# Optimization experiments

Hardware: AMD Instinct MI355X
Metric: run time of the kernel (lower is better)

## Reference

```python
import jax, jax.numpy as jnp
import numpy as np

L, D, H, NP, PS, C, OUT, N = 8, 768, 12, 14, 16, 3, 1000, 32
DH = D // H
S = NP * NP + 1  # 197 tokens (cls + patches)
EPS = 1e-5


def pos_embeddings(seq_len, d):
    # result[i,j] = sin(i/10000^(j/d)) if j even else cos(i/10000^((j-1)/d))
    i = np.arange(seq_len)[:, None].astype(np.float64)
    j = np.arange(d)[None, :]
    ang = i / (10000.0 ** ((j - (j % 2)) / d))
    pe = np.where(j % 2 == 0, np.sin(ang), np.cos(ang))
    return jnp.asarray(pe, dtype=jnp.float32)


def setup_inputs() -> dict:
    key = jax.random.key(0)
    ks = jax.random.split(key, 16)
    s = 0.02
    return {
        'images': jax.random.normal(ks[0], (N, C, NP * PS, NP * PS), jnp.float32),
        'Wm': jax.random.normal(ks[1], (C * PS * PS, D), jnp.float32) * s,
        'bm': jnp.zeros((D,), jnp.float32),
        'cls_tok': jax.random.uniform(ks[2], (1, D), jnp.float32),
        'pos_emb': pos_embeddings(S, D),
        'ln1_w': jnp.ones((L, D), jnp.float32),
        'ln1_b': jnp.zeros((L, D), jnp.float32),
        'Wq': jax.random.normal(ks[3], (L, H, DH, DH), jnp.float32) * s,
        'bq': jnp.zeros((L, H, DH), jnp.float32),
        'Wk': jax.random.normal(ks[4], (L, H, DH, DH), jnp.float32) * s,
        'bk': jnp.zeros((L, H, DH), jnp.float32),
        'Wv': jax.random.normal(ks[5], (L, H, DH, DH), jnp.float32) * s,
        'bv': jnp.zeros((L, H, DH), jnp.float32),
        'ln2_w': jnp.ones((L, D), jnp.float32),
        'ln2_b': jnp.zeros((L, D), jnp.float32),
        'W1': jax.random.normal(ks[6], (L, D, 4 * D), jnp.float32) * s,
        'b1': jnp.zeros((L, 4 * D), jnp.float32),
        'W2': jax.random.normal(ks[7], (L, 4 * D, D), jnp.float32) * s,
        'b2': jnp.zeros((L, D), jnp.float32),
        'Wout': jax.random.normal(ks[8], (D, OUT), jnp.float32) * s,
        'bout': jnp.zeros((OUT,), jnp.float32),
    }


def layernorm(x, w, b):
    mu = x.mean(-1, keepdims=True)
    var = ((x - mu) ** 2).mean(-1, keepdims=True)
    return (x - mu) * jax.lax.rsqrt(var + EPS) * w + b


def vit_forward(images, Wm, bm, cls_tok, pos_emb, ln1_w, ln1_b, Wq, bq, Wk, bk, Wv, bv,
                ln2_w, ln2_b, W1, b1, W2, b2, Wout, bout):
    n = images.shape[0]
    # patchify: (n,c,h,w) -> (n, NP*NP, C*PS*PS), each patch flattened in (c,ph,pw) order
    patches = images.reshape(n, C, NP, PS, NP, PS).transpose(0, 2, 4, 1, 3, 5)
    patches = patches.reshape(n, NP * NP, C * PS * PS)
    tokens = patches @ Wm + bm                                   # [n, S-1, D]
    tokens = jnp.concatenate([jnp.broadcast_to(cls_tok, (n, 1, D)), tokens], axis=1)
    out = tokens + pos_emb                                       # [n, S, D]

    scale = 1.0 / jnp.sqrt(jnp.asarray(DH, jnp.float32))

    def block(x, p):
        l1w, l1b, wq, bq_, wk, bk_, wv, bv_, l2w, l2b, w1, b1_, w2, b2_ = p
        h = layernorm(x, l1w, l1b).reshape(n, S, H, DH)
        q = jnp.einsum('nshd,hde->nshe', h, wq) + bq_
        k = jnp.einsum('nshd,hde->nshe', h, wk) + bk_
        v = jnp.einsum('nshd,hde->nshe', h, wv) + bv_
        att = jax.nn.softmax(jnp.einsum('nshe,nthe->nhst', q, k) * scale, axis=-1)
        o = jnp.einsum('nhst,nthe->nshe', att, v).reshape(n, S, D)
        x = x + o
        h2 = layernorm(x, l2w, l2b)
        x = x + (jax.nn.gelu(h2 @ w1 + b1_, approximate=False) @ w2 + b2_)
        return x, None

    out, _ = jax.lax.scan(block, out, (ln1_w, ln1_b, Wq, bq, Wk, bk, Wv, bv,
                                       ln2_w, ln2_b, W1, b1, W2, b2))
    cls = out[:, 0]                                              # [n, D]
    return jax.nn.softmax(cls @ Wout + bout, axis=-1)            # [n, OUT]


def reference(images, Wm, bm, cls_tok, pos_emb, ln1_w, ln1_b, Wq, bq, Wk, bk, Wv, bv,
              ln2_w, ln2_b, W1, b1, W2, b2, Wout, bout):
    return vit_forward(images, Wm, bm, cls_tok, pos_emb, ln1_w, ln1_b, Wq, bq, Wk, bk,
                       Wv, bv, ln2_w, ln2_b, W1, b1, W2, b2, Wout, bout)
```

## Files before the change

kernel.cpp:

```cpp
#include <hip/hip_runtime.h>
#include <math.h>

#define N_ 32
#define S_ 197
#define D_ 768
#define H_ 12
#define L_ 8
#define FF_ 3072
#define MTOK (N_ * S_)
#define ND (N_ * S_ * D_)

typedef __attribute__((ext_vector_type(8))) short short8x;
typedef __attribute__((ext_vector_type(4))) float floatx4;
typedef unsigned short ushort_t;
typedef unsigned int uint_t;

__device__ __forceinline__ ushort_t f2bf_rn(float x) {
  uint_t u = __float_as_uint(x);
  uint_t r = (u + 0x7fff + ((u >> 16) & 1)) >> 16;
  return (ushort_t)r;
}
__device__ __forceinline__ float bf2f(ushort_t h) {
  return __uint_as_float(((uint_t)h) << 16);
}

__global__ __launch_bounds__(256) void patchify_kernel(const float* __restrict__ img,
                                                       ushort_t* __restrict__ phi,
                                                       ushort_t* __restrict__ plo) {
  int idx = blockIdx.x * 256 + threadIdx.x;
  if (idx >= 6272 * 768) return;
  int mp = idx / 768, kk = idx - mp * 768;
  int n = mp / 196, p = mp - n * 196;
  int py = p / 14, px = p - py * 14;
  int c = kk >> 8, r = kk & 255;
  int u = r >> 4, vv = r & 15;
  float val = img[((size_t)(n * 3 + c) * 224 + py * 16 + u) * 224 + px * 16 + vv];
  ushort_t hi = f2bf_rn(val);
  phi[idx] = hi;
  plo[idx] = f2bf_rn(val - bf2f(hi));
}

__global__ __launch_bounds__(256) void cls_init_kernel(const float* __restrict__ cls_tok,
                                                       const float* __restrict__ pos,
                                                       float* __restrict__ x) {
  int idx = blockIdx.x * 256 + threadIdx.x;
  int n = idx / 768, d = idx - n * 768;
  x[(size_t)n * S_ * D_ + d] = cls_tok[d] + pos[d];
}

__global__ __launch_bounds__(256) void wconvert_kernel(const float* __restrict__ W,
                                                       ushort_t* __restrict__ Thi,
                                                       ushort_t* __restrict__ Tlo, int K, int N) {
  __shared__ float T[32][36];
  int n0 = blockIdx.x * 32, k0 = blockIdx.y * 32;
  int t = threadIdx.x;
  int r = t >> 3, c4 = (t & 7) * 4;
  float4 v = *(const float4*)&W[(size_t)(k0 + r) * N + n0 + c4];
  T[c4 + 0][r] = v.x;
  T[c4 + 1][r] = v.y;
  T[c4 + 2][r] = v.z;
  T[c4 + 3][r] = v.w;
  __syncthreads();
  ushort4 hi, lo;
  float a;
  a = T[r][c4 + 0]; hi.x = f2bf_rn(a); lo.x = f2bf_rn(a - bf2f(hi.x));
  a = T[r][c4 + 1]; hi.y = f2bf_rn(a); lo.y = f2bf_rn(a - bf2f(hi.y));
  a = T[r][c4 + 2]; hi.z = f2bf_rn(a); lo.z = f2bf_rn(a - bf2f(hi.z));
  a = T[r][c4 + 3]; hi.w = f2bf_rn(a); lo.w = f2bf_rn(a - bf2f(hi.w));
  size_t o = (size_t)(n0 + r) * K + k0 + c4;
  *(ushort4*)&Thi[o] = hi;
  *(ushort4*)&Tlo[o] = lo;
}

#define EPI_PATCH 1
#define EPI_GELU 2
#define EPI_ATOM 3
#define LDST 40

template <int EPI, int KP>
__global__ __launch_bounds__(256) void gemm_mfma(
    const ushort_t* __restrict__ Ahi, const ushort_t* __restrict__ Alo,
    const ushort_t* __restrict__ Bhi, const ushort_t* __restrict__ Blo,
    const float* __restrict__ bias, float* __restrict__ Cf, ushort_t* __restrict__ Chi,
    ushort_t* __restrict__ Clo, int M, int K, int Nc, const float* __restrict__ pos) {
  __shared__ ushort_t As[2][128 * LDST];
  __shared__ ushort_t Bs[2][128 * LDST];
  int tid = threadIdx.x;
  int wave = tid >> 6, lane = tid & 63;
  int wr = (wave >> 1) * 64, wc = (wave & 1) * 64;
  int q = lane >> 4, l15 = lane & 15;
  int m0 = blockIdx.x * 128, n0 = blockIdx.y * 128;
  int kbeg = (KP > 1) ? blockIdx.z * (K / KP) : 0;
  int kend = kbeg + K / KP;

  floatx4 acc[4][4];
#pragma unroll
  for (int i = 0; i < 4; ++i)
#pragma unroll
    for (int j = 0; j < 4; ++j)
#pragma unroll
      for (int e = 0; e < 4; ++e) acc[i][j][e] = 0.f;

  int sr = tid >> 2;
  int kq = tid & 3;

  for (int k0 = kbeg; k0 < kend; k0 += 32) {
#pragma unroll
    for (int it = 0; it < 2; ++it) {
      int rr = it * 64 + sr;
      int gm = m0 + rr;
      if (gm > M - 1) gm = M - 1;
      size_t aoff = (size_t)gm * K + k0 + kq * 8;
      *(uint4*)&As[0][rr * LDST + kq * 8] = *(const uint4*)&Ahi[aoff];
      *(uint4*)&As[1][rr * LDST + kq * 8] = *(const uint4*)&Alo[aoff];
      size_t boff = (size_t)(n0 + rr) * K + k0 + kq * 8;
      *(uint4*)&Bs[0][rr * LDST + kq * 8] = *(const uint4*)&Bhi[boff];
      *(uint4*)&Bs[1][rr * LDST + kq * 8] = *(const uint4*)&Blo[boff];
    }
    __syncthreads();
    short8x ah[4], al[4], bh[4], bl[4];
    int abase = (wr + l15) * LDST + q * 8;
    int bbase = (wc + l15) * LDST + q * 8;
#pragma unroll
    for (int i = 0; i < 4; ++i) {
      ah[i] = *(const short8x*)&As[0][abase + i * 16 * LDST];
      al[i] = *(const short8x*)&As[1][abase + i * 16 * LDST];
      bh[i] = *(const short8x*)&Bs[0][bbase + i * 16 * LDST];
      bl[i] = *(const short8x*)&Bs[1][bbase + i * 16 * LDST];
    }
#pragma unroll
    for (int i = 0; i < 4; ++i)
#pragma unroll
      for (int j = 0; j < 4; ++j) {
        acc[i][j] = __builtin_amdgcn_mfma_f32_16x16x32_bf16(ah[i], bh[j], acc[i][j], 0, 0, 0);
        acc[i][j] = __builtin_amdgcn_mfma_f32_16x16x32_bf16(ah[i], bl[j], acc[i][j], 0, 0, 0);
        acc[i][j] = __builtin_amdgcn_mfma_f32_16x16x32_bf16(al[i], bh[j], acc[i][j], 0, 0, 0);
      }
    __syncthreads();
  }

#pragma unroll
  for (int i = 0; i < 4; ++i) {
#pragma unroll
    for (int j = 0; j < 4; ++j) {
      int col = n0 + wc + j * 16 + l15;
#pragma unroll
      for (int r4 = 0; r4 < 4; ++r4) {
        int gr = m0 + wr + i * 16 + q * 4 + r4;
        if (gr >= M) continue;
        if (EPI == EPI_ATOM) {
          float v = acc[i][j][r4];
          if (KP == 1 || blockIdx.z == 0) v += bias[col];
          unsafeAtomicAdd(&Cf[(size_t)gr * 768 + col], v);
        } else {
          float v = acc[i][j][r4] + bias[col];
          if (EPI == EPI_PATCH) {
            int n = gr / 196, t = gr - n * 196 + 1;
            Cf[((size_t)n * S_ + t) * 768 + col] = v + pos[(size_t)t * 768 + col];
          } else {
            float g = 0.5f * v * (1.f + erff(v * 0.70710678118654752f));
            ushort_t hi = f2bf_rn(g);
            size_t o = (size_t)gr * FF_ + col;
            Chi[o] = hi;
            Clo[o] = f2bf_rn(g - bf2f(hi));
          }
        }
      }
    }
  }
}

__global__ __launch_bounds__(256) void ln_kernel(const float* __restrict__ x,
                                                 ushort_t* __restrict__ hhi,
                                                 ushort_t* __restrict__ hlo,
                                                 const float* __restrict__ w,
                                                 const float* __restrict__ b) {
  int tok = blockIdx.x * 4 + (threadIdx.x >> 6);
  int lane = threadIdx.x & 63;
  const float* xr = x + (size_t)tok * 768;
  float4 v[3];
  float s = 0.f, s2 = 0.f;
#pragma unroll
  for (int i = 0; i < 3; ++i) {
    v[i] = *(const float4*)&xr[i * 256 + lane * 4];
    s += v[i].x + v[i].y + v[i].z + v[i].w;
    s2 += v[i].x * v[i].x + v[i].y * v[i].y + v[i].z * v[i].z + v[i].w * v[i].w;
  }
#pragma unroll
  for (int m = 32; m > 0; m >>= 1) { s += __shfl_xor(s, m, 64); s2 += __shfl_xor(s2, m, 64); }
  float mu = s * (1.f / 768.f);
  float var = s2 * (1.f / 768.f) - mu * mu;
  float rs = rsqrtf(var + 1e-5f);
#pragma unroll
  for (int i = 0; i < 3; ++i) {
    float4 wv = *(const float4*)&w[i * 256 + lane * 4];
    float4 bv = *(const float4*)&b[i * 256 + lane * 4];
    float o0 = (v[i].x - mu) * rs * wv.x + bv.x;
    float o1 = (v[i].y - mu) * rs * wv.y + bv.y;
    float o2 = (v[i].z - mu) * rs * wv.z + bv.z;
    float o3 = (v[i].w - mu) * rs * wv.w + bv.w;
    ushort4 oh, ol;
    oh.x = f2bf_rn(o0); ol.x = f2bf_rn(o0 - bf2f(oh.x));
    oh.y = f2bf_rn(o1); ol.y = f2bf_rn(o1 - bf2f(oh.y));
    oh.z = f2bf_rn(o2); ol.z = f2bf_rn(o2 - bf2f(oh.z));
    oh.w = f2bf_rn(o3); ol.w = f2bf_rn(o3 - bf2f(oh.w));
    size_t o = (size_t)tok * 768 + i * 256 + lane * 4;
    *(ushort4*)&hhi[o] = oh;
    *(ushort4*)&hlo[o] = ol;
  }
}

#define KSTR 72

__global__ __launch_bounds__(256) void qkv_mfma(
    const ushort_t* __restrict__ hhi, const ushort_t* __restrict__ hlo,
    const float* __restrict__ Wq, const float* __restrict__ Wk, const float* __restrict__ Wv,
    const float* __restrict__ bq, const float* __restrict__ bk, const float* __restrict__ bv,
    ushort_t* __restrict__ qhi, ushort_t* __restrict__ qlo, ushort_t* __restrict__ khi,
    ushort_t* __restrict__ klo, ushort_t* __restrict__ vhi, ushort_t* __restrict__ vlo) {
  __shared__ ushort_t As[2][128 * KSTR];
  __shared__ ushort_t Ws[2][64 * KSTR];
  int tid = threadIdx.x;
  int wave = tid >> 6, lane = tid & 63;
  int q = lane >> 4, l15 = lane & 15;
  int m0 = blockIdx.x * 128, h = blockIdx.y;
  int wm = wave >> 1, wj = wave & 1;

#pragma unroll
  for (int p = 0; p < 2; ++p) {
    const ushort_t* src = p == 0 ? hhi : hlo;
#pragma unroll
    for (int it = 0; it < 4; ++it) {
      int idx = it * 256 + tid;
      int r = idx >> 3, c = idx & 7;
      int gm = m0 + r;
      if (gm > MTOK - 1) gm = MTOK - 1;
      *(uint4*)&As[p][r * KSTR + c * 8] = *(const uint4*)&src[(size_t)gm * 768 + h * 64 + c * 8];
    }
  }

  const float* Wmat[3] = {Wq + (size_t)h * 4096, Wk + (size_t)h * 4096, Wv + (size_t)h * 4096};
  const float* Bmat[3] = {bq + h * 64, bk + h * 64, bv + h * 64};
  ushort_t* Ohi[3] = {qhi, khi, vhi};
  ushort_t* Olo[3] = {qlo, klo, vlo};

  for (int mat = 0; mat < 3; ++mat) {
    __syncthreads();
#pragma unroll
    for (int it = 0; it < 4; ++it) {
      int idx = it * 256 + tid;
      int r = idx >> 4, c4 = (idx & 15) * 4;
      float4 wv = *(const float4*)&Wmat[mat][r * 64 + c4];
      float vals[4] = {wv.x, wv.y, wv.z, wv.w};
#pragma unroll
      for (int i = 0; i < 4; ++i) {
        ushort_t hi = f2bf_rn(vals[i]);
        Ws[0][(c4 + i) * KSTR + r] = hi;
        Ws[1][(c4 + i) * KSTR + r] = f2bf_rn(vals[i] - bf2f(hi));
      }
    }
    __syncthreads();

    floatx4 acc[4][2];
#pragma unroll
    for (int i = 0; i < 4; ++i)
#pragma unroll
      for (int j = 0; j < 2; ++j)
#pragma unroll
        for (int e = 0; e < 4; ++e) acc[i][j][e] = 0.f;

#pragma unroll
    for (int ks = 0; ks < 2; ++ks) {
      short8x bh[2], bl[2];
#pragma unroll
      for (int j = 0; j < 2; ++j) {
        int bb = (wj * 32 + j * 16 + l15) * KSTR + ks * 32 + q * 8;
        bh[j] = *(const short8x*)&Ws[0][bb];
        bl[j] = *(const short8x*)&Ws[1][bb];
      }
#pragma unroll
      for (int i = 0; i < 4; ++i) {
        int ab = (wm * 64 + i * 16 + l15) * KSTR + ks * 32 + q * 8;
        short8x ah = *(const short8x*)&As[0][ab];
        short8x al = *(const short8x*)&As[1][ab];
#pragma unroll
        for (int j = 0; j < 2; ++j) {
          acc[i][j] = __builtin_amdgcn_mfma_f32_16x16x32_bf16(ah, bh[j], acc[i][j], 0, 0, 0);
          acc[i][j] = __builtin_amdgcn_mfma_f32_16x16x32_bf16(ah, bl[j], acc[i][j], 0, 0, 0);
          acc[i][j] = __builtin_amdgcn_mfma_f32_16x16x32_bf16(al, bh[j], acc[i][j], 0, 0, 0);
        }
      }
    }
#pragma unroll
    for (int i = 0; i < 4; ++i)
#pragma unroll
      for (int j = 0; j < 2; ++j) {
        int col = wj * 32 + j * 16 + l15;
        float bias = Bmat[mat][col];
#pragma unroll
        for (int r = 0; r < 4; ++r) {
          int tok = m0 + wm * 64 + i * 16 + q * 4 + r;
          if (tok >= MTOK) continue;
          float v = acc[i][j][r] + bias;
          ushort_t hi = f2bf_rn(v);
          size_t o = (size_t)tok * 768 + h * 64 + col;
          Ohi[mat][o] = hi;
          Olo[mat][o] = f2bf_rn(v - bf2f(hi));
        }
      }
  }
}

__global__ __launch_bounds__(256) void attn_mfma(
    const ushort_t* __restrict__ qhi, const ushort_t* __restrict__ qlo,
    const ushort_t* __restrict__ khi, const ushort_t* __restrict__ klo,
    const ushort_t* __restrict__ vhi, const ushort_t* __restrict__ vlo,
    float* __restrict__ X) {
  __shared__ ushort_t Qs[2][64 * KSTR];
  __shared__ ushort_t Ks[2][64 * KSTR];
  __shared__ ushort_t Vs[2][64 * KSTR];
  int tid = threadIdx.x;
  int wave = tid >> 6, lane = tid & 63;
  int q = lane >> 4, l15 = lane & 15;
  int qc = blockIdx.x, h = blockIdx.y, n = blockIdx.z;
  int q0 = qc * 64;
  int row0 = wave * 16;

#pragma unroll
  for (int p = 0; p < 2; ++p) {
    const ushort_t* src = p == 0 ? qhi : qlo;
#pragma unroll
    for (int it = 0; it < 2; ++it) {
      int idx = it * 256 + tid;
      int r = idx >> 3, c = idx & 7;
      int gr = q0 + r;
      if (gr > S_ - 1) gr = S_ - 1;
      *(uint4*)&Qs[p][r * KSTR + c * 8] =
          *(const uint4*)&src[((size_t)n * S_ + gr) * 768 + h * 64 + c * 8];
    }
  }
  __syncthreads();
  short8x qa_h[2], qa_l[2];
#pragma unroll
  for (int ks = 0; ks < 2; ++ks) {
    int ab = (row0 + l15) * KSTR + ks * 32 + q * 8;
    qa_h[ks] = *(const short8x*)&Qs[0][ab];
    qa_l[ks] = *(const short8x*)&Qs[1][ab];
  }

  float mrow[4], lrow[4];
  floatx4 oa[4];
#pragma unroll
  for (int r = 0; r < 4; ++r) { mrow[r] = -INFINITY; lrow[r] = 0.f; }
#pragma unroll
  for (int j = 0; j < 4; ++j)
#pragma unroll
    for (int e = 0; e < 4; ++e) oa[j][e] = 0.f;

  for (int t = 0; t < 4; ++t) {
    __syncthreads();
#pragma unroll
    for (int p = 0; p < 2; ++p) {
      const ushort_t* src = p == 0 ? khi : klo;
#pragma unroll
      for (int it = 0; it < 2; ++it) {
        int idx = it * 256 + tid;
        int r = idx >> 3, c = idx & 7;
        int gk = t * 64 + r;
        if (gk > S_ - 1) gk = S_ - 1;
        *(uint4*)&Ks[p][r * KSTR + c * 8] =
            *(const uint4*)&src[((size_t)n * S_ + gk) * 768 + h * 64 + c * 8];
      }
    }
    {
      int d = tid & 63, kg = tid >> 6;
#pragma unroll
      for (int p = 0; p < 2; ++p) {
        const ushort_t* src = p == 0 ? vhi : vlo;
#pragma unroll
        for (int k4 = 0; k4 < 4; ++k4) {
          ushort4 pk;
          ushort_t tmp[4];
#pragma unroll
          for (int i = 0; i < 4; ++i) {
            int gk = t * 64 + kg * 16 + k4 * 4 + i;
            if (gk > S_ - 1) gk = S_ - 1;
            tmp[i] = src[((size_t)n * S_ + gk) * 768 + h * 64 + d];
          }
          pk.x = tmp[0]; pk.y = tmp[1]; pk.z = tmp[2]; pk.w = tmp[3];
          *(ushort4*)&Vs[p][d * KSTR + kg * 16 + k4 * 4] = pk;
        }
      }
    }
    __syncthreads();

    floatx4 sc[4];
#pragma unroll
    for (int j = 0; j < 4; ++j) {
#pragma unroll
      for (int e = 0; e < 4; ++e) sc[j][e] = 0.f;
#pragma unroll
      for (int ks = 0; ks < 2; ++ks) {
        int bb = (j * 16 + l15) * KSTR + ks * 32 + q * 8;
        short8x kb_h = *(const short8x*)&Ks[0][bb];
        short8x kb_l = *(const short8x*)&Ks[1][bb];
        sc[j] = __builtin_amdgcn_mfma_f32_16x16x32_bf16(qa_h[ks], kb_h, sc[j], 0, 0, 0);
        sc[j] = __builtin_amdgcn_mfma_f32_16x16x32_bf16(qa_h[ks], kb_l, sc[j], 0, 0, 0);
        sc[j] = __builtin_amdgcn_mfma_f32_16x16x32_bf16(qa_l[ks], kb_h, sc[j], 0, 0, 0);
      }
    }
    __syncthreads();

    bool kvalid[4];
#pragma unroll
    for (int j = 0; j < 4; ++j) kvalid[j] = (t * 64 + j * 16 + l15) < S_;
#pragma unroll
    for (int r = 0; r < 4; ++r) {
      float sv[4];
#pragma unroll
      for (int j = 0; j < 4; ++j) sv[j] = kvalid[j] ? sc[j][r] * 0.125f : -INFINITY;
      float mx = fmaxf(fmaxf(sv[0], sv[1]), fmaxf(sv[2], sv[3]));
#pragma unroll
      for (int msk = 1; msk < 16; msk <<= 1) mx = fmaxf(mx, __shfl_xor(mx, msk, 64));
      float mn = fmaxf(mrow[r], mx);
      float al = expf(mrow[r] - mn);
      float p[4], ps = 0.f;
#pragma unroll
      for (int j = 0; j < 4; ++j) { p[j] = expf(sv[j] - mn); ps += p[j]; }
#pragma unroll
      for (int msk = 1; msk < 16; msk <<= 1) ps += __shfl_xor(ps, msk, 64);
      lrow[r] = lrow[r] * al + ps;
      mrow[r] = mn;
#pragma unroll
      for (int j = 0; j < 4; ++j) oa[j][r] *= al;
      int prow = (row0 + q * 4 + r) * KSTR;
#pragma unroll
      for (int j = 0; j < 4; ++j) {
        ushort_t phv = f2bf_rn(p[j]);
        Ks[0][prow + j * 16 + l15] = phv;
        Ks[1][prow + j * 16 + l15] = f2bf_rn(p[j] - bf2f(phv));
      }
    }

#pragma unroll
    for (int ks = 0; ks < 2; ++ks) {
      int ab = (row0 + l15) * KSTR + ks * 32 + q * 8;
      short8x pa_h = *(const short8x*)&Ks[0][ab];
      short8x pa_l = *(const short8x*)&Ks[1][ab];
#pragma unroll
      for (int j = 0; j < 4; ++j) {
        int bb = (j * 16 + l15) * KSTR + ks * 32 + q * 8;
        short8x vb_h = *(const short8x*)&Vs[0][bb];
        short8x vb_l = *(const short8x*)&Vs[1][bb];
        oa[j] = __builtin_amdgcn_mfma_f32_16x16x32_bf16(pa_h, vb_h, oa[j], 0, 0, 0);
        oa[j] = __builtin_amdgcn_mfma_f32_16x16x32_bf16(pa_h, vb_l, oa[j], 0, 0, 0);
        oa[j] = __builtin_amdgcn_mfma_f32_16x16x32_bf16(pa_l, vb_h, oa[j], 0, 0, 0);
      }
    }
  }

#pragma unroll
  for (int r = 0; r < 4; ++r) {
    int row = q0 + row0 + q * 4 + r;
    if (row >= S_) continue;
    float invl = 1.f / lrow[r];
#pragma unroll
    for (int j = 0; j < 4; ++j)
      X[((size_t)n * S_ + row) * 768 + h * 64 + j * 16 + l15] += oa[j][r] * invl;
  }
}

__global__ __launch_bounds__(256) void head_kernel(const float* __restrict__ x,
                                                   const float* __restrict__ Wout,
                                                   const float* __restrict__ bout,
                                                   float* __restrict__ out) {
  __shared__ float cls[768];
  __shared__ float red[4];
  int n = blockIdx.x, tid = threadIdx.x;
  int w = tid >> 6, lane = tid & 63;
  for (int d = tid; d < 768; d += 256) cls[d] = x[(size_t)n * S_ * D_ + d];
  __syncthreads();
  int j0 = tid * 4;
  bool act = j0 < 1000;
  float a0 = 0.f, a1 = 0.f, a2 = 0.f, a3 = 0.f;
  if (act) {
    for (int kk = 0; kk < 768; ++kk) {
      float c = cls[kk];
      float4 wv = *(const float4*)&Wout[(size_t)kk * 1000 + j0];
      a0 += c * wv.x;
      a1 += c * wv.y;
      a2 += c * wv.z;
      a3 += c * wv.w;
    }
    a0 += bout[j0];
    a1 += bout[j0 + 1];
    a2 += bout[j0 + 2];
    a3 += bout[j0 + 3];
  }
  float mx = act ? fmaxf(fmaxf(a0, a1), fmaxf(a2, a3)) : -INFINITY;
#pragma unroll
  for (int m = 32; m > 0; m >>= 1) mx = fmaxf(mx, __shfl_xor(mx, m, 64));
  if (lane == 0) red[w] = mx;
  __syncthreads();
  mx = fmaxf(fmaxf(red[0], red[1]), fmaxf(red[2], red[3]));
  __syncthreads();
  float e0 = 0.f, e1 = 0.f, e2 = 0.f, e3 = 0.f, ss = 0.f;
  if (act) {
    e0 = expf(a0 - mx);
    e1 = expf(a1 - mx);
    e2 = expf(a2 - mx);
    e3 = expf(a3 - mx);
    ss = e0 + e1 + e2 + e3;
  }
#pragma unroll
  for (int m = 32; m > 0; m >>= 1) ss += __shfl_xor(ss, m, 64);
  if (lane == 0) red[w] = ss;
  __syncthreads();
  ss = red[0] + red[1] + red[2] + red[3];
  if (act) {
    float inv = 1.f / ss;
    out[(size_t)n * 1000 + j0] = e0 * inv;
    out[(size_t)n * 1000 + j0 + 1] = e1 * inv;
    out[(size_t)n * 1000 + j0 + 2] = e2 * inv;
    out[(size_t)n * 1000 + j0 + 3] = e3 * inv;
  }
}

extern "C" void kernel_launch(void* const* d_in, const int* in_sizes, int n_in, void* d_out,
                              int out_size, void* d_ws, size_t ws_size, hipStream_t stream) {
  const float* images = (const float*)d_in[0];
  const float* Wm = (const float*)d_in[1];
  const float* bm = (const float*)d_in[2];
  const float* cls_tok = (const float*)d_in[3];
  const float* pos_emb = (const float*)d_in[4];
  const float* ln1_w = (const float*)d_in[5];
  const float* ln1_b = (const float*)d_in[6];
  const float* Wq = (const float*)d_in[7];
  const float* bq = (const float*)d_in[8];
  const float* Wk = (const float*)d_in[9];
  const float* bk = (const float*)d_in[10];
  const float* Wv = (const float*)d_in[11];
  const float* bv = (const float*)d_in[12];
  const float* ln2_w = (const float*)d_in[13];
  const float* ln2_b = (const float*)d_in[14];
  const float* W1 = (const float*)d_in[15];
  const float* b1 = (const float*)d_in[16];
  const float* W2 = (const float*)d_in[17];
  const float* b2 = (const float*)d_in[18];
  const float* Wout = (const float*)d_in[19];
  const float* bout = (const float*)d_in[20];
  float* out = (float*)d_out;

  char* base = (char*)d_ws;
  float* x = (float*)base;
  ushort_t* hhi = (ushort_t*)(base + (size_t)ND * 4);
  ushort_t* hlo = hhi + (size_t)ND;
  char* R = base + (size_t)ND * 8;
  ushort_t* qhi = (ushort_t*)R;
  ushort_t* qlo = qhi + (size_t)ND;
  ushort_t* khi = qlo + (size_t)ND;
  ushort_t* klo = khi + (size_t)ND;
  ushort_t* vhi = klo + (size_t)ND;
  ushort_t* vlo = vhi + (size_t)ND;
  ushort_t* ghi = (ushort_t*)R;
  ushort_t* glo = ghi + (size_t)MTOK * FF_;
  ushort_t* phi = (ushort_t*)R;
  ushort_t* plo = phi + (size_t)6272 * 768;
  char* WB = R + (size_t)MTOK * FF_ * 4;
  ushort_t* w1hi = (ushort_t*)WB;
  ushort_t* w1lo = w1hi + (size_t)768 * FF_;
  ushort_t* w2hi = w1lo + (size_t)768 * FF_;
  ushort_t* w2lo = w2hi + (size_t)768 * FF_;

  patchify_kernel<<<(6272 * 768 + 255) / 256, 256, 0, stream>>>(images, phi, plo);
  wconvert_kernel<<<dim3(24, 24), 256, 0, stream>>>(Wm, w1hi, w1lo, 768, 768);
  gemm_mfma<EPI_PATCH, 1><<<dim3(49, 6), 256, 0, stream>>>(phi, plo, w1hi, w1lo, bm, x,
                                                           nullptr, nullptr, 6272, 768, 768,
                                                           pos_emb);
  cls_init_kernel<<<(32 * 768) / 256, 256, 0, stream>>>(cls_tok, pos_emb, x);

  for (int l = 0; l < 8; ++l) {
    ln_kernel<<<MTOK / 4, 256, 0, stream>>>(x, hhi, hlo, ln1_w + l * 768, ln1_b + l * 768);
    qkv_mfma<<<dim3(50, 12), 256, 0, stream>>>(
        hhi, hlo, Wq + (size_t)l * 49152, Wk + (size_t)l * 49152, Wv + (size_t)l * 49152,
        bq + l * 768, bk + l * 768, bv + l * 768, qhi, qlo, khi, klo, vhi, vlo);
    attn_mfma<<<dim3(4, 12, 32), 256, 0, stream>>>(qhi, qlo, khi, klo, vhi, vlo, x);
    ln_kernel<<<MTOK / 4, 256, 0, stream>>>(x, hhi, hlo, ln2_w + l * 768, ln2_b + l * 768);
    wconvert_kernel<<<dim3(96, 24), 256, 0, stream>>>(W1 + (size_t)l * 768 * FF_, w1hi, w1lo,
                                                      768, FF_);
    gemm_mfma<EPI_GELU, 1><<<dim3(50, 24), 256, 0, stream>>>(hhi, hlo, w1hi, w1lo, b1 + l * FF_,
                                                             nullptr, ghi, glo, MTOK, 768, FF_,
                                                             nullptr);
    wconvert_kernel<<<dim3(24, 96), 256, 0, stream>>>(W2 + (size_t)l * FF_ * 768, w2hi, w2lo,
                                                      FF_, 768);
    gemm_mfma<EPI_ATOM, 2><<<dim3(50, 6, 2), 256, 0, stream>>>(ghi, glo, w2hi, w2lo,
                                                               b2 + l * 768, x, nullptr,
                                                               nullptr, MTOK, FF_, 768,
                                                               nullptr);
  }
  head_kernel<<<32, 256, 0, stream>>>(x, Wout, bout, out);
}
```

Measured before the change: 3.914 ms.

## Load GEMM tiles via direct global-to-LDS loads with XOR-swizzled layout

Replaces the register-staged global loads and LDS stores in the split-bf16 MFMA GEMM with global_load_lds 16-byte direct-to-LDS transfers. Because those transfers write contiguously per wave, the padded row stride is dropped and bank conflicts are avoided with an XOR swizzle on the 8-element chunk index, applied on both the load and read sides. The aim is to save VGPRs and instructions in the load path and shrink LDS use. The loop remains single-buffered and waits on vmcnt(0) before the barrier, so the load latency is still exposed.

Measured after the change: 3.409 ms. -12.9%, faster.

```diff
diff --git a/kernel.cpp b/kernel.cpp
--- a/kernel.cpp
+++ b/kernel.cpp
@@ -22,6 +22,11 @@
 }
 __device__ __forceinline__ float bf2f(ushort_t h) {
   return __uint_as_float(((uint_t)h) << 16);
+}
+
+__device__ __forceinline__ void gload16(const ushort_t* g, ushort_t* l) {
+  __builtin_amdgcn_global_load_lds((const __attribute__((address_space(1))) void*)g,
+                                   (__attribute__((address_space(3))) void*)l, 16, 0, 0);
 }
 
 __global__ __launch_bounds__(256) void patchify_kernel(const float* __restrict__ img,
@@ -75,7 +80,6 @@
 #define EPI_PATCH 1
 #define EPI_GELU 2
 #define EPI_ATOM 3
-#define LDST 40
 
 template <int EPI, int KP>
 __global__ __launch_bounds__(256) void gemm_mfma(
@@ -83,8 +87,8 @@
     const ushort_t* __restrict__ Bhi, const ushort_t* __restrict__ Blo,
     const float* __restrict__ bias, float* __restrict__ Cf, ushort_t* __restrict__ Chi,
     ushort_t* __restrict__ Clo, int M, int K, int Nc, const float* __restrict__ pos) {
-  __shared__ ushort_t As[2][128 * LDST];
-  __shared__ ushort_t Bs[2][128 * LDST];
+  __shared__ ushort_t As[2][128 * 32];
+  __shared__ ushort_t Bs[2][128 * 32];
   int tid = threadIdx.x;
   int wave = tid >> 6, lane = tid & 63;
   int wr = (wave >> 1) * 64, wc = (wave & 1) * 64;
@@ -101,32 +105,37 @@
 #pragma unroll
       for (int e = 0; e < 4; ++e) acc[i][j][e] = 0.f;
 
-  int sr = tid >> 2;
-  int kq = tid & 3;
+  int srow_in = lane >> 2;
+  int schunk = lane & 3;
+  int csw = (q ^ ((l15 >> 1) & 3)) * 8;
 
   for (int k0 = kbeg; k0 < kend; k0 += 32) {
 #pragma unroll
-    for (int it = 0; it < 2; ++it) {
-      int rr = it * 64 + sr;
-      int gm = m0 + rr;
+    for (int j = 0; j < 2; ++j) {
+      int rbase = (wave << 5) + (j << 4);
+      int r = rbase + srow_in;
+      int cc = schunk ^ ((r >> 1) & 3);
+      int gm = m0 + r;
       if (gm > M - 1) gm = M - 1;
-      size_t aoff = (size_t)gm * K + k0 + kq * 8;
-      *(uint4*)&As[0][rr * LDST + kq * 8] = *(const uint4*)&Ahi[aoff];
-      *(uint4*)&As[1][rr * LDST + kq * 8] = *(const uint4*)&Alo[aoff];
-      size_t boff = (size_t)(n0 + rr) * K + k0 + kq * 8;
-      *(uint4*)&Bs[0][rr * LDST + kq * 8] = *(const uint4*)&Bhi[boff];
-      *(uint4*)&Bs[1][rr * LDST + kq * 8] = *(const uint4*)&Blo[boff];
-    }
+      size_t aoff = (size_t)gm * K + k0 + cc * 8;
+      size_t boff = (size_t)(n0 + r) * K + k0 + cc * 8;
+      gload16(&Ahi[aoff], &As[0][rbase * 32]);
+      gload16(&Alo[aoff], &As[1][rbase * 32]);
+      gload16(&Bhi[boff], &Bs[0][rbase * 32]);
+      gload16(&Blo[boff], &Bs[1][rbase * 32]);
+    }
+    asm volatile("s_waitcnt vmcnt(0)" ::: "memory");
     __syncthreads();
+
     short8x ah[4], al[4], bh[4], bl[4];
-    int abase = (wr + l15) * LDST + q * 8;
-    int bbase = (wc + l15) * LDST + q * 8;
 #pragma unroll
     for (int i = 0; i < 4; ++i) {
-      ah[i] = *(const short8x*)&As[0][abase + i * 16 * LDST];
-      al[i] = *(const short8x*)&As[1][abase + i * 16 * LDST];
-      bh[i] = *(const short8x*)&Bs[0][bbase + i * 16 * LDST];
-      bl[i] = *(const short8x*)&Bs[1][bbase + i * 16 * LDST];
+      int ao = (wr + i * 16 + l15) * 32 + csw;
+      int bo = (wc + i * 16 + l15) * 32 + csw;
+      ah[i] = *(const short8x*)&As[0][ao];
+      al[i] = *(const short8x*)&As[1][ao];
+      bh[i] = *(const short8x*)&Bs[0][bo];
+      bl[i] = *(const short8x*)&Bs[1][bo];
     }
 #pragma unroll
     for (int i = 0; i < 4; ++i)
```
